# Kernel tuning notes

Measured on AMD Instinct MI355X. Metric: run time of the kernel, lower is better.

The kernel has to match this reference:

```python
import jax, jax.numpy as jnp
import numpy as np
import math

CHANNELS, BINS, HEADS, KSIZE = 4, 1024, 8, 3
ROT_DIM = BINS // HEADS // 2  # 64: rotate first half of each 128-dim head


def _rope(t):
    # t: [b, c, heads, w, d]; rotate first ROT_DIM dims, interleaved-pair style
    w = t.shape[-2]
    inv_freq = 1.0 / (10000.0 ** (jnp.arange(0, ROT_DIM, 2, dtype=jnp.float32) / ROT_DIM))
    freqs = jnp.arange(w, dtype=jnp.float32)[:, None] * inv_freq[None, :]   # [w, ROT_DIM//2]
    freqs = jnp.repeat(freqs, 2, axis=-1)                                    # [w, ROT_DIM]
    cos, sin = jnp.cos(freqs), jnp.sin(freqs)
    t_rot, t_pass = t[..., :ROT_DIM], t[..., ROT_DIM:]
    pair = t_rot.reshape(t_rot.shape[:-1] + (ROT_DIM // 2, 2))
    rotated = jnp.stack((-pair[..., 1], pair[..., 0]), axis=-1).reshape(t_rot.shape)
    return jnp.concatenate([t_rot * cos + rotated * sin, t_pass], axis=-1)


def _proj(x, w_lin, w_conv, b_conv):
    # MultichannelLinear: contract last dim with per-channel [out, in] weight
    y = jnp.einsum('bchi,coi->bcho', x, w_lin)
    # depthwise Conv2d, kernel (1, 3), padding (0, 1), groups = channels
    y = jax.lax.conv_general_dilated(
        y, w_conv, window_strides=(1, 1), padding=((0, 0), (1, 1)),
        dimension_numbers=('NCHW', 'OIHW', 'NCHW'), feature_group_count=CHANNELS)
    return y + b_conv[None, :, None, None]


def _split_heads(y):
    b, c, h, w = y.shape
    # transpose(2,3) -> [b,c,w,h]; reshape -> [b,c,w,heads,d]; permute -> [b,c,heads,w,d]
    return y.transpose(0, 1, 3, 2).reshape(b, c, w, HEADS, h // HEADS).transpose(0, 1, 3, 2, 4)


def setup_inputs() -> dict:
    key = jax.random.key(0)
    k1, k2, k3, k4, k5 = jax.random.split(key, 5)
    s_lin = 1.0 / math.sqrt(BINS)
    x = jax.random.normal(k1, (2, CHANNELS, BINS, BINS), dtype=jnp.float32)
    w_q_lin = jax.random.uniform(k2, (CHANNELS, BINS, BINS), jnp.float32, -s_lin, s_lin)
    w_q_conv = jax.random.uniform(k3, (CHANNELS, 1, 1, KSIZE), jnp.float32, -0.5, 0.5)
    b_q_conv = jax.random.uniform(k4, (CHANNELS,), jnp.float32, -0.5, 0.5)
    w_out = jax.random.uniform(k5, (CHANNELS, BINS, BINS), jnp.float32, -s_lin, s_lin)
    return {"x": x, "w_q_lin": w_q_lin, "w_q_conv": w_q_conv, "b_q_conv": b_q_conv, "w_out": w_out}


def reference(x, w_q_lin, w_q_conv, b_q_conv, w_out):
    b, c, h, w = x.shape
    # NOTE: original forward uses self.q_proj for q, k AND v (k_proj/v_proj unused)
    p = _proj(x, w_q_lin, w_q_conv, b_q_conv)          # [b,c,h,w]
    ph = _split_heads(p)                                # [b,c,heads,w,d]
    q = _rope(ph)
    k = _rope(ph)
    v = ph
    qk = jnp.einsum('bcnqd,bcnkd->bcnqk', q, k) / math.sqrt(h)
    a = jnp.einsum('bcnqk,bcnkd->bcnqd', jax.nn.softmax(qk, axis=-1), v)
    # merge heads back: [b,c,heads,w,d] -> [b,c,w,h] -> [b,c,h,w]
    a = a.transpose(0, 1, 3, 2, 4).reshape(b, c, w, h).transpose(0, 1, 3, 2)
    return jnp.einsum('bchi,coi->bcho', a, w_out)
```

## Files before the change

### kernel.cpp

```cpp
#include <hip/hip_runtime.h>
#include <cstdint>
#include <cstddef>

typedef __bf16 bf16;
typedef bf16 bf16x2 __attribute__((ext_vector_type(2)));
typedef bf16 bf16x4 __attribute__((ext_vector_type(4)));
typedef bf16 bf16x8 __attribute__((ext_vector_type(8)));
typedef float f32x4 __attribute__((ext_vector_type(4)));
typedef float f32x16 __attribute__((ext_vector_type(16)));

union B2F { float f; bf16x2 h; };

__device__ __forceinline__ void gload_lds16(const bf16* g, bf16* l) {
    __builtin_amdgcn_global_load_lds(
        (__attribute__((address_space(1))) void*)(uintptr_t)(g),
        (__attribute__((address_space(3))) void*)(l),
        16, 0, 0);
}

__global__ __launch_bounds__(256) void cvt3_kernel(const float* __restrict__ a,
                                                   bf16* __restrict__ oa, int na4,
                                                   const float* __restrict__ b,
                                                   bf16* __restrict__ ob, int nb4,
                                                   const float* __restrict__ c,
                                                   bf16* __restrict__ oc, int nc4) {
    int i = blockIdx.x * 256 + threadIdx.x;
    const float* in; bf16* out;
    if (i < na4) { in = a; out = oa; }
    else if (i < na4 + nb4) { in = b; out = ob; i -= na4; }
    else if (i < na4 + nb4 + nc4) { in = c; out = oc; i -= na4 + nb4; }
    else return;
    float4 v = ((const float4*)in)[i];
    bf16x4 o;
    o[0] = (bf16)v.x; o[1] = (bf16)v.y; o[2] = (bf16)v.z; o[3] = (bf16)v.w;
    *(bf16x4*)(out + (size_t)i * 4) = o;
}

__global__ __launch_bounds__(256) void rope_tab_kernel(float2* __restrict__ t) {
    int i = blockIdx.x * 256 + threadIdx.x;
    int w = i >> 5, j = i & 31;
    float inv = exp2f(-(float)j * (13.287712379549449f / 32.0f));
    float a = (float)w * inv;
    t[i] = make_float2(cosf(a), sinf(a));
}

template <bool F32OUT>
__global__ void __launch_bounds__(256) gemm_bt(const bf16* __restrict__ A,
                                               const bf16* __restrict__ B,
                                               void* __restrict__ Cout) {
    __shared__ alignas(16) bf16 As[128 * 64];
    __shared__ alignas(16) bf16 Bs[128 * 64];
    const int tid = threadIdx.x, lane = tid & 63, wave = tid >> 6;
    const int l15 = lane & 15, quad = lane >> 4;
    const int b = blockIdx.x;
    const int s = b & 7, mt = (b >> 3) & 7, nt = b >> 6;
    const bf16* Ab = A + ((size_t)s << 20) + (size_t)mt * 128 * 1024;
    const bf16* Bb = B + ((size_t)(s & 3) << 20) + (size_t)nt * 128 * 1024;
    const int wm = (wave >> 1) * 64, wn = (wave & 1) * 64;

    const f32x4 fzero = {0.f, 0.f, 0.f, 0.f};
    f32x4 acc[4][4];
    for (int i = 0; i < 4; ++i)
        for (int j = 0; j < 4; ++j) acc[i][j] = fzero;

    const int sr = wave * 8 + (lane >> 3);
    const int sc = (lane & 7) * 8;

    for (int kt = 0; kt < 16; ++kt) {
        __syncthreads();
        for (int it = 0; it < 4; ++it) {
            int r = it * 32 + sr;
            gload_lds16(Ab + (size_t)r * 1024 + kt * 64 + sc, As + r * 64 + sc);
            gload_lds16(Bb + (size_t)r * 1024 + kt * 64 + sc, Bs + r * 64 + sc);
        }
        __syncthreads();
        for (int kk = 0; kk < 2; ++kk) {
            bf16x8 af[4], bfr[4];
            for (int i = 0; i < 4; ++i)
                af[i] = *(const bf16x8*)(As + (wm + i * 16 + l15) * 64 + kk * 32 + quad * 8);
            for (int j = 0; j < 4; ++j)
                bfr[j] = *(const bf16x8*)(Bs + (wn + j * 16 + l15) * 64 + kk * 32 + quad * 8);
            for (int i = 0; i < 4; ++i)
                for (int j = 0; j < 4; ++j)
                    acc[i][j] = __builtin_amdgcn_mfma_f32_16x16x32_bf16(af[i], bfr[j],
                                                                        acc[i][j], 0, 0, 0);
        }
    }
    size_t cbase = ((size_t)s << 20) + (size_t)mt * 128 * 1024 + (size_t)nt * 128;
    for (int i = 0; i < 4; ++i)
        for (int j = 0; j < 4; ++j) {
            int m = wm + i * 16 + quad * 4;
            int n = wn + j * 16 + l15;
            for (int r = 0; r < 4; ++r) {
                float v = acc[i][j][r];
                if (F32OUT)
                    ((float*)Cout)[cbase + (size_t)(m + r) * 1024 + n] = v;
                else
                    ((bf16*)Cout)[cbase + (size_t)(m + r) * 1024 + n] = (bf16)v;
            }
        }
}

__global__ void __launch_bounds__(256) conv_rope_kernel(
    const bf16* __restrict__ Yb, const float* __restrict__ wconv,
    const float* __restrict__ bconv, bf16* __restrict__ Qhat,
    bf16* __restrict__ Vhat, const float2* __restrict__ rtab) {
    __shared__ float Pt[32][260];
    const int s = blockIdx.z, cch = s & 3;
    const int h0 = blockIdx.y * 32, w0 = blockIdx.x * 256;
    const bf16* Y = Yb + ((size_t)s << 20);
    const float k0 = wconv[cch * 3], k1 = wconv[cch * 3 + 1], k2 = wconv[cch * 3 + 2];
    const float bias = bconv[cch];
    const float SQS = 0.21233045f;

    for (int it = 0; it < 4; ++it) {
        const int hh = threadIdx.x >> 3;
        const int wseg = (threadIdx.x & 7) + it * 8;
        const int h = h0 + hh, w = w0 + wseg * 8;
        const bf16* yrow = Y + ((size_t)h << 10);
        bf16x8 yv = *(const bf16x8*)(yrow + w);
        float yc[10];
        yc[0] = (w > 0) ? (float)yrow[w - 1] : 0.f;
        for (int i = 0; i < 8; ++i) yc[i + 1] = (float)yv[i];
        yc[9] = (w + 8 < 1024) ? (float)yrow[w + 8] : 0.f;
        bf16x8 pb;
        for (int i = 0; i < 8; ++i) {
            float p = fmaf(k0, yc[i], fmaf(k1, yc[i + 1], fmaf(k2, yc[i + 2], bias)));
            Pt[hh][wseg * 8 + i] = p;
            pb[i] = (bf16)p;
        }
        const int head = h >> 7, d = h & 127;
        *(bf16x8*)(Vhat + ((((size_t)s * 8 + head) * 128 + (w >> 3)) << 10) + d * 8) = pb;
    }
    __syncthreads();
    {
        const int dcb = threadIdx.x >> 6;
        const int head = h0 >> 7;
        const int d0 = (h0 & 127) + dcb * 8;
        const int hb0 = dcb * 8;
        for (int it = 0; it < 4; ++it) {
            const int wl = (threadIdx.x & 63) + it * 64;
            const int w = w0 + wl;
            float q[8];
            if (d0 < 64) {
                for (int j = 0; j < 8; j += 2) {
                    float2 cs = rtab[(w << 5) + ((d0 + j) >> 1)];
                    float a = Pt[hb0 + j][wl], b = Pt[hb0 + j + 1][wl];
                    q[j]     = fmaf(a, cs.x, -b * cs.y);
                    q[j + 1] = fmaf(b, cs.x,  a * cs.y);
                }
            } else {
                for (int j = 0; j < 8; ++j) q[j] = Pt[hb0 + j][wl];
            }
            bf16x8 qb;
            for (int j = 0; j < 8; ++j) qb[j] = (bf16)(q[j] * SQS);
            *(bf16x8*)(Qhat + ((((size_t)s * 8 + head) * 16 + (d0 >> 3)) << 13) +
                       (size_t)w * 8) = qb;
        }
    }
}

__global__ void __launch_bounds__(256, 2) attn_kernel(const bf16* __restrict__ Qhat,
                                                      const bf16* __restrict__ Vhat,
                                                      bf16* __restrict__ AO) {
    __shared__ alignas(16) char smem[66048];
    const int tid = threadIdx.x, lane = tid & 63, wave = tid >> 6;
    const int l31 = lane & 31, h = lane >> 5;
    const int b = blockIdx.x;
    const int sh = b & 63, qtile = b >> 6;
    const int s = sh >> 3, head = sh & 7, q0 = qtile * 128;
    const bf16* Qg = Qhat + (size_t)sh * 131072;
    const bf16* Vg = Vhat + (size_t)sh * 131072;

    const int myq = q0 + wave * 32 + l31;
    bf16x8 qf[8];
    for (int ks8 = 0; ks8 < 8; ++ks8)
        qf[ks8] = *(const bf16x8*)(Qg + (size_t)(ks8 * 2 + h) * 8192 + (size_t)myq * 8);

    f32x16 Oacc[4];
    for (int nt = 0; nt < 4; ++nt)
        for (int e = 0; e < 16; ++e) Oacc[nt][e] = 0.f;
    float lsum = 0.f;

    auto stage = [&](int kt, int buf) {
        bf16* Ks = (bf16*)(smem + buf * 32768);
        bf16* Vs = Ks + 8192;
        for (int t = 0; t < 4; ++t) {
            int dc = wave * 4 + t;
            gload_lds16(Qg + (size_t)dc * 8192 + (size_t)(kt * 64 + lane) * 8,
                        Ks + (dc * 64 + lane) * 8);
            int wc = dc >> 1, half = dc & 1;
            gload_lds16(Vg + (size_t)(kt * 8 + wc) * 1024 + (size_t)(half * 64 + lane) * 8,
                        Vs + (wc * 128 + half * 64 + lane) * 8);
        }
    };

    stage(0, 0);
    for (int kt = 0; kt < 16; ++kt) {
        __syncthreads();
        if (kt < 15) stage(kt + 1, (kt + 1) & 1);
        bf16* Ks = (bf16*)(smem + (kt & 1) * 32768);
        bf16* Vs = Ks + 8192;

        f32x16 st[2];
        for (int e = 0; e < 16; ++e) { st[0][e] = 0.f; st[1][e] = 0.f; }
        for (int ks8 = 0; ks8 < 8; ++ks8) {
            bf16x8 kf0 = *(const bf16x8*)(Ks + ((ks8 * 2 + h) * 64 + l31) * 8);
            bf16x8 kf1 = *(const bf16x8*)(Ks + ((ks8 * 2 + h) * 64 + 32 + l31) * 8);
            st[0] = __builtin_amdgcn_mfma_f32_32x32x16_bf16(kf0, qf[ks8], st[0], 0, 0, 0);
            st[1] = __builtin_amdgcn_mfma_f32_32x32x16_bf16(kf1, qf[ks8], st[1], 0, 0, 0);
        }

        float pk[2][8], pkx[2][8];
        float lacc = 0.f;
        for (int mt = 0; mt < 2; ++mt)
            for (int k = 0; k < 8; ++k) {
                float a = exp2f(st[mt][2 * k]);
                float c = exp2f(st[mt][2 * k + 1]);
                lacc += a + c;
                B2F u; u.h = bf16x2{(bf16)a, (bf16)c};
                pk[mt][k] = u.f;
            }
        lsum += lacc;
        for (int mt = 0; mt < 2; ++mt)
            for (int k = 0; k < 8; ++k) pkx[mt][k] = __shfl_xor(pk[mt][k], 32);

        for (int ks = 0; ks < 4; ++ks) {
            const int bb = ks & 1, mt = ks >> 1;
            bf16x8 pf;
            float* pfF = (float*)&pf;
            pfF[0] = h ? pkx[mt][4 * bb + 2] : pk[mt][4 * bb + 0];
            pfF[1] = h ? pkx[mt][4 * bb + 3] : pk[mt][4 * bb + 1];
            pfF[2] = h ? pk[mt][4 * bb + 2] : pkx[mt][4 * bb + 0];
            pfF[3] = h ? pk[mt][4 * bb + 3] : pkx[mt][4 * bb + 1];
            for (int nt = 0; nt < 4; ++nt) {
                bf16x8 vf = *(const bf16x8*)(Vs + ((ks * 2 + h) * 128 + nt * 32 + l31) * 8);
                Oacc[nt] = __builtin_amdgcn_mfma_f32_32x32x16_bf16(pf, vf, Oacc[nt], 0, 0, 0);
            }
        }
    }

    lsum += __shfl_xor(lsum, 32);
    float* lsf = (float*)(smem + 65536) + wave * 32;
    if (lane < 32) lsf[lane] = 1.0f / lsum;
    f32x4 rv[4];
    __builtin_amdgcn_s_waitcnt(0);
    for (int rg = 0; rg < 4; ++rg)
        rv[rg] = *(const f32x4*)(lsf + 8 * rg + 4 * h);

    __syncthreads();
    bf16* Ot = (bf16*)smem;
    for (int nt = 0; nt < 4; ++nt) {
        int d = nt * 32 + l31;
        for (int rg = 0; rg < 4; ++rg) {
            int q = wave * 32 + 8 * rg + 4 * h;
            bf16x4 o4;
            for (int e = 0; e < 4; ++e)
                o4[e] = (bf16)(Oacc[nt][rg * 4 + e] * rv[rg][e]);
            *(bf16x4*)(Ot + d * 136 + q) = o4;
        }
    }
    __syncthreads();
    bf16* AOg = AO + ((size_t)s << 20);
    for (int it = 0; it < 8; ++it) {
        int d = it * 16 + (tid >> 4);
        int qc = (tid & 15) * 8;
        bf16x8 v = *(const bf16x8*)(Ot + d * 136 + qc);
        *(bf16x8*)(AOg + (size_t)(head * 128 + d) * 1024 + q0 + qc) = v;
    }
}

extern "C" void kernel_launch(void* const* d_in, const int* in_sizes, int n_in,
                              void* d_out, int out_size, void* d_ws, size_t ws_size,
                              hipStream_t stream) {
    const float* x  = (const float*)d_in[0];
    const float* wq = (const float*)d_in[1];
    const float* wc = (const float*)d_in[2];
    const float* bc = (const float*)d_in[3];
    const float* wo = (const float*)d_in[4];
    float* out = (float*)d_out;

    char* ws = (char*)d_ws;
    bf16* xb   = (bf16*)ws;
    bf16* wqb  = (bf16*)(ws + (16u << 20));
    bf16* wob  = (bf16*)(ws + (24u << 20));
    bf16* Yb   = (bf16*)(ws + (32u << 20));
    bf16* Qhat = (bf16*)(ws + (48u << 20));
    bf16* Vhat = (bf16*)(ws + (64u << 20));
    float2* rtab = (float2*)(ws + (80u << 20));
    bf16* AO   = xb;

    cvt3_kernel<<<16384, 256, 0, stream>>>(x, xb, 2097152, wq, wqb, 1048576,
                                           wo, wob, 1048576);
    rope_tab_kernel<<<128, 256, 0, stream>>>(rtab);

    gemm_bt<false><<<512, 256, 0, stream>>>(xb, wqb, Yb);
    conv_rope_kernel<<<dim3(4, 32, 8), 256, 0, stream>>>(Yb, wc, bc, Qhat, Vhat, rtab);
    attn_kernel<<<512, 256, 0, stream>>>(Qhat, Vhat, AO);
    gemm_bt<true><<<512, 256, 0, stream>>>(AO, wob, out);
}
```

Before: 222.6 us.

## Permute V layout so softmax probabilities feed PV MFMA without lane shuffles

The V tensor is now written in an interleaved layout in which each 16-key group is split into two 4-element halves placed 1024 elements apart. This lets the exp'd score accumulator registers be packed directly into bf16x8 A-operands for the PV MFMA, removing the 16 cross-lane shuffles and the select logic per key tile. The cost is two 8-byte stores instead of one 16-byte store in the projection epilogue, and correctness depends on the new V layout matching the register order of the MFMA accumulator.

```diff
diff --git a/kernel.cpp b/kernel.cpp
--- a/kernel.cpp
+++ b/kernel.cpp
@@ -8,8 +8,6 @@
 typedef bf16 bf16x8 __attribute__((ext_vector_type(8)));
 typedef float f32x4 __attribute__((ext_vector_type(4)));
 typedef float f32x16 __attribute__((ext_vector_type(16)));
-
-union B2F { float f; bf16x2 h; };
 
 __device__ __forceinline__ void gload_lds16(const bf16* g, bf16* l) {
     __builtin_amdgcn_global_load_lds(
@@ -130,7 +128,12 @@
             pb[i] = (bf16)p;
         }
         const int head = h >> 7, d = h & 127;
-        *(bf16x8*)(Vhat + ((((size_t)s * 8 + head) * 128 + (w >> 3)) << 10) + d * 8) = pb;
+        size_t vb = ((((size_t)s * 8 + head) * 128 + (w >> 4) * 2) << 10) + d * 8 +
+                    ((w >> 3) & 1) * 4;
+        bf16x4 lo = {pb[0], pb[1], pb[2], pb[3]};
+        bf16x4 hi = {pb[4], pb[5], pb[6], pb[7]};
+        *(bf16x4*)(Vhat + vb) = lo;
+        *(bf16x4*)(Vhat + vb + 1024) = hi;
     }
     __syncthreads();
     {
@@ -211,28 +214,24 @@
             st[1] = __builtin_amdgcn_mfma_f32_32x32x16_bf16(kf1, qf[ks8], st[1], 0, 0, 0);
         }
 
-        float pk[2][8], pkx[2][8];
+        bf16x8 pfr[4];
         float lacc = 0.f;
         for (int mt = 0; mt < 2; ++mt)
-            for (int k = 0; k < 8; ++k) {
-                float a = exp2f(st[mt][2 * k]);
-                float c = exp2f(st[mt][2 * k + 1]);
-                lacc += a + c;
-                B2F u; u.h = bf16x2{(bf16)a, (bf16)c};
-                pk[mt][k] = u.f;
+            for (int hh = 0; hh < 2; ++hh) {
+                bf16x8 pf;
+                for (int e = 0; e < 8; e += 2) {
+                    float a = exp2f(st[mt][hh * 8 + e]);
+                    float c = exp2f(st[mt][hh * 8 + e + 1]);
+                    lacc += a + c;
+                    pf[e] = (bf16)a;
+                    pf[e + 1] = (bf16)c;
+                }
+                pfr[mt * 2 + hh] = pf;
             }
         lsum += lacc;
-        for (int mt = 0; mt < 2; ++mt)
-            for (int k = 0; k < 8; ++k) pkx[mt][k] = __shfl_xor(pk[mt][k], 32);
 
         for (int ks = 0; ks < 4; ++ks) {
-            const int bb = ks & 1, mt = ks >> 1;
-            bf16x8 pf;
-            float* pfF = (float*)&pf;
-            pfF[0] = h ? pkx[mt][4 * bb + 2] : pk[mt][4 * bb + 0];
-            pfF[1] = h ? pkx[mt][4 * bb + 3] : pk[mt][4 * bb + 1];
-            pfF[2] = h ? pk[mt][4 * bb + 2] : pkx[mt][4 * bb + 0];
-            pfF[3] = h ? pk[mt][4 * bb + 3] : pkx[mt][4 * bb + 1];
+            const bf16x8 pf = pfr[ks];
             for (int nt = 0; nt < 4; ++nt) {
                 bf16x8 vf = *(const bf16x8*)(Vs + ((ks * 2 + h) * 128 + nt * 32 + l31) * 8);
                 Oacc[nt] = __builtin_amdgcn_mfma_f32_32x32x16_bf16(pf, vf, Oacc[nt], 0, 0, 0);
```

After: 220.9 us. Within noise of the previous version (-0.8%).
